# Optimization experiments

Measured on AMD Instinct MI355X. Metric: run time of the kernel, lower is better.

## Reference

```python
import jax, jax.numpy as jnp
import numpy as np

TWO_PI = 2.0 * np.pi


def _grid_sample(w, g):
    """Bilinear sample. w: [M,C,H,W]; g: [M,2,H,W] coords in [-1,1] (x,y),
    align_corners=True, border-clamped."""
    H, W = w.shape[-2], w.shape[-1]
    x = (g[:, 0] + 1.0) * 0.5 * (W - 1)  # [M,H,W]
    y = (g[:, 1] + 1.0) * 0.5 * (H - 1)
    x0 = jnp.floor(x)
    y0 = jnp.floor(y)
    fx = x - x0
    fy = y - y0
    x0i = jnp.clip(x0.astype(jnp.int32), 0, W - 1)
    x1i = jnp.clip(x0i + 1, 0, W - 1)
    y0i = jnp.clip(y0.astype(jnp.int32), 0, H - 1)
    y1i = jnp.clip(y0i + 1, 0, H - 1)

    def samp(wm, yi, xi):
        return wm[:, yi, xi]  # [C,H,W]

    v00 = jax.vmap(samp)(w, y0i, x0i)
    v01 = jax.vmap(samp)(w, y0i, x1i)
    v10 = jax.vmap(samp)(w, y1i, x0i)
    v11 = jax.vmap(samp)(w, y1i, x1i)
    fx = fx[:, None]  # broadcast over channel dim
    fy = fy[:, None]
    return (1 - fy) * ((1 - fx) * v00 + fx * v01) + fy * ((1 - fx) * v10 + fx * v11)


def _forward(in_H, out_H, weight, grid_H, grid_Rn, mask):
    No, Ni = out_H.shape[0], in_H.shape[0]
    N = grid_H.shape[0]
    Gk, Cout, Cin, kh, kw = weight.shape

    # inverse_H: angles negate; left_apply_to_H: angles add (pairwise)
    out_inv = -out_H  # [No,1]
    theta = (out_inv[:, None, 0] + in_H[None, :, 0]).reshape(-1)  # [No*Ni]

    # interpolate_H: periodic linear interp over uniform angle grid
    step = TWO_PI / N
    pos = jnp.mod(theta, TWO_PI) / step
    i0 = jnp.floor(pos).astype(jnp.int32) % N
    i1 = (i0 + 1) % N
    frac = (pos - jnp.floor(pos))[:, None]
    wflat = weight.reshape(Gk, -1)  # [Gk, Cout*Cin*kh*kw]
    w = (1.0 - frac) * wflat[i0] + frac * wflat[i1]  # [No*Ni, C]
    w = w.reshape(No * Ni, Cin * Cout, kh, kw)

    # left_apply_to_Rn: rotate spatial grid by out_H^{-1}
    ang = out_inv[:, 0]
    c, s = jnp.cos(ang), jnp.sin(ang)
    gx = c[:, None, None] * grid_Rn[0] - s[:, None, None] * grid_Rn[1]
    gy = s[:, None, None] * grid_Rn[0] + c[:, None, None] * grid_Rn[1]
    grids = jnp.stack([gx, gy], axis=1)  # [No,2,kh,kw]
    grids = jnp.repeat(grids, Ni, axis=0)  # repeat_interleave -> [No*Ni,2,kh,kw]

    # interpolate_Rn: bilinear grid sample
    w = _grid_sample(w, grids)  # [No*Ni, Cin*Cout, kh, kw]
    w = w.reshape(No, Ni, Cin, Cout, kh, kw)
    # .transpose(0,3).transpose(1,3) -> [Cout, No, Cin, Ni, kh, kw]
    w = jnp.transpose(w, (3, 0, 2, 1, 4, 5))
    return mask * w


def setup_inputs() -> dict:
    key = jax.random.key(0)
    k1, k2, k3 = jax.random.split(key, 3)
    N, Cout, Cin, ks = 8, 128, 128, 5
    in_H = jax.random.uniform(k1, (N, 1), dtype=jnp.float32) * TWO_PI
    out_H = jax.random.uniform(k2, (N, 1), dtype=jnp.float32) * TWO_PI
    fan_in = Cin * ks * ks
    weight = jax.random.normal(k3, (N, Cout, Cin, ks, ks), dtype=jnp.float32) / np.sqrt(fan_in)
    grid_H = (jnp.arange(N) * (TWO_PI / N)).astype(jnp.float32)
    lin = jnp.linspace(-1.0, 1.0, ks)
    X, Y = jnp.meshgrid(lin, lin, indexing='xy')
    grid_Rn = jnp.stack([X, Y]).astype(jnp.float32)  # [2, ks, ks]
    mask = (X ** 2 + Y ** 2 <= 1.0 + 1e-6).astype(jnp.float32)  # circular mask
    return dict(in_H=in_H, out_H=out_H, weight=weight, grid_H=grid_H,
                grid_Rn=grid_Rn, mask=mask)


def reference(in_H, out_H, weight, grid_H, grid_Rn, mask):
    return _forward(in_H, out_H, weight, grid_H, grid_Rn, mask)
```

## Files before the change

### kernel.cpp

```cpp
#include <hip/hip_runtime.h>
#include <math.h>


#define TWO_PI_F 6.28318530717958647692f

__global__ __launch_bounds__(256) void rotconv_weight_kernel(
    const float* __restrict__ in_H,
    const float* __restrict__ out_H,
    const float* __restrict__ weight,
    const float* __restrict__ grid_Rn,
    const float* __restrict__ mask,
    float* __restrict__ out)
{
    __shared__ __align__(16) float s_tile[256 * 25];
    __shared__ int4   s_off[25];
    __shared__ float4 s_w[25];

    const int t  = threadIdx.x;
    const int bx = blockIdx.x;
    const int vt = bx & 7;
    const int ut = (bx >> 3) & 7;
    const int i  = (bx >> 6) & 7;
    const int o  = bx >> 9;
    const int u0 = ut * 16;
    const int v0 = vt * 16;

    const float ang = -out_H[o];

    const float theta = in_H[i] + ang;
    float m = fmodf(theta, TWO_PI_F);
    if (m < 0.0f) m += TWO_PI_F;
    const float pos  = m * (8.0f / TWO_PI_F);
    const float pf   = floorf(pos);
    const float frac = pos - pf;
    const int g0 = ((int)pf) & 7;
    const int g1 = (g0 + 1) & 7;
    const float om = 1.0f - frac;

    if (t < 25) {
        const int k = t;
        float sthe, cthe;
        sincosf(ang, &sthe, &cthe);
        const float X = grid_Rn[k];
        const float Y = grid_Rn[25 + k];
        const float gx = cthe * X - sthe * Y;
        const float gy = sthe * X + cthe * Y;
        const float x = (gx + 1.0f) * 2.0f;
        const float y = (gy + 1.0f) * 2.0f;
        const float x0f = floorf(x);
        const float y0f = floorf(y);
        const float fx = x - x0f;
        const float fy = y - y0f;
        int x0 = (int)x0f; x0 = x0 < 0 ? 0 : (x0 > 4 ? 4 : x0);
        int y0 = (int)y0f; y0 = y0 < 0 ? 0 : (y0 > 4 ? 4 : y0);
        const int x1 = x0 + 1 > 4 ? 4 : x0 + 1;
        const int y1 = y0 + 1 > 4 ? 4 : y0 + 1;
        const float mk = mask[k];
        s_off[k] = make_int4(y0 * 5 + x0, y0 * 5 + x1, y1 * 5 + x0, y1 * 5 + x1);
        s_w[k] = make_float4(mk * (1.0f - fy) * (1.0f - fx),
                             mk * (1.0f - fy) * fx,
                             mk * fy * (1.0f - fx),
                             mk * fy * fx);
    }

    const size_t b0 = ((size_t)(g0 * 128 + u0) * 128 + v0) * 25;
    const size_t b1 = ((size_t)(g1 * 128 + u0) * 128 + v0) * 25;
    for (int f4 = t; f4 < 1600; f4 += 256) {
        const int chunk = f4 / 100;
        const int off4  = f4 - chunk * 100;
        const size_t a  = (size_t)chunk * 3200 + (size_t)off4 * 4;
        const float4 a0 = *reinterpret_cast<const float4*>(weight + b0 + a);
        const float4 a1 = *reinterpret_cast<const float4*>(weight + b1 + a);
        float4 bl;
        bl.x = om * a0.x + frac * a1.x;
        bl.y = om * a0.y + frac * a1.y;
        bl.z = om * a0.z + frac * a1.z;
        bl.w = om * a0.w + frac * a1.w;
        *reinterpret_cast<float4*>(s_tile + (size_t)f4 * 4) = bl;
    }

    __syncthreads();

    const int uu = t >> 4;
    const int vv = t & 15;
    const float* tp = s_tile + t * 25;
    const size_t ob = ((((size_t)(v0 + vv) * 8 + o) * 128 + (u0 + uu)) * 8 + i) * 25;

#pragma unroll
    for (int k = 0; k < 25; ++k) {
        const int4   of = s_off[k];
        const float4 w  = s_w[k];
        out[ob + k] = w.x * tp[of.x] + w.y * tp[of.y]
                    + w.z * tp[of.z] + w.w * tp[of.w];
    }
}

extern "C" void kernel_launch(void* const* d_in, const int* in_sizes, int n_in,
                              void* d_out, int out_size, void* d_ws, size_t ws_size,
                              hipStream_t stream) {
    const float* in_H    = (const float*)d_in[0];
    const float* out_H   = (const float*)d_in[1];
    const float* weight  = (const float*)d_in[2];
    const float* grid_Rn = (const float*)d_in[4];
    const float* mask    = (const float*)d_in[5];
    float* out = (float*)d_out;

    rotconv_weight_kernel<<<dim3(4096), dim3(256), 0, stream>>>(
        in_H, out_H, weight, grid_Rn, mask, out);
}
```

Measured before the change: 159.2 us.

## Remap output phase so threads own one tap and write contiguous runs

Each thread now handles a single kernel tap k, computing its bilinear offsets and weights in registers instead of using shared-memory tables. Groups of 25 threads then walk the (u,v) runs, so consecutive lanes write consecutive output floats, replacing the old pattern where each thread wrote 25 elements with a 25-float stride. The x1 clamp is folded into the weights so loads are adjacent pairs. Only 250 of 256 threads take part in the output phase, and each run index needs about 26 iterations.

New measurement: 145.1 us. 1.1x faster.

```diff
diff --git a/kernel.cpp b/kernel.cpp
--- a/kernel.cpp
+++ b/kernel.cpp
@@ -13,8 +13,6 @@
     float* __restrict__ out)
 {
     __shared__ __align__(16) float s_tile[256 * 25];
-    __shared__ int4   s_off[25];
-    __shared__ float4 s_w[25];
 
     const int t  = threadIdx.x;
     const int bx = blockIdx.x;
@@ -37,8 +35,11 @@
     const int g1 = (g0 + 1) & 7;
     const float om = 1.0f - frac;
 
-    if (t < 25) {
-        const int k = t;
+    const int grp = t / 25;
+    const int k   = t - grp * 25;
+    int rb0, rb1;
+    float w00, w01, w10, w11;
+    {
         float sthe, cthe;
         sincosf(ang, &sthe, &cthe);
         const float X = grid_Rn[k];
@@ -53,14 +54,17 @@
         const float fy = y - y0f;
         int x0 = (int)x0f; x0 = x0 < 0 ? 0 : (x0 > 4 ? 4 : x0);
         int y0 = (int)y0f; y0 = y0 < 0 ? 0 : (y0 > 4 ? 4 : y0);
-        const int x1 = x0 + 1 > 4 ? 4 : x0 + 1;
         const int y1 = y0 + 1 > 4 ? 4 : y0 + 1;
         const float mk = mask[k];
-        s_off[k] = make_int4(y0 * 5 + x0, y0 * 5 + x1, y1 * 5 + x0, y1 * 5 + x1);
-        s_w[k] = make_float4(mk * (1.0f - fy) * (1.0f - fx),
-                             mk * (1.0f - fy) * fx,
-                             mk * fy * (1.0f - fx),
-                             mk * fy * fx);
+        float wa = mk * (1.0f - fy) * (1.0f - fx);
+        float wb = mk * (1.0f - fy) * fx;
+        float wc = mk * fy * (1.0f - fx);
+        float wd = mk * fy * fx;
+        int xb = x0;
+        if (x0 == 4) { xb = 3; wb += wa; wa = 0.0f; wd += wc; wc = 0.0f; }
+        rb0 = y0 * 5 + xb;
+        rb1 = y1 * 5 + xb;
+        w00 = wa; w01 = wb; w10 = wc; w11 = wd;
     }
 
     const size_t b0 = ((size_t)(g0 * 128 + u0) * 128 + v0) * 25;
@@ -81,17 +85,20 @@
 
     __syncthreads();
 
-    const int uu = t >> 4;
-    const int vv = t & 15;
-    const float* tp = s_tile + t * 25;
-    const size_t ob = ((((size_t)(v0 + vv) * 8 + o) * 128 + (u0 + uu)) * 8 + i) * 25;
-
-#pragma unroll
-    for (int k = 0; k < 25; ++k) {
-        const int4   of = s_off[k];
-        const float4 w  = s_w[k];
-        out[ob + k] = w.x * tp[of.x] + w.y * tp[of.y]
-                    + w.z * tp[of.z] + w.w * tp[of.w];
+    const size_t obase = ((((size_t)v0 * 8 + o) * 128 + u0) * 8 + i) * 25 + k;
+    if (grp < 10) {
+#pragma unroll 4
+        for (int run = grp; run < 256; run += 10) {
+            const int uu = run >> 4;
+            const int vv = run & 15;
+            const float* tp = s_tile + run * 25;
+            const float v00 = tp[rb0];
+            const float v01 = tp[rb0 + 1];
+            const float v10 = tp[rb1];
+            const float v11 = tp[rb1 + 1];
+            out[obase + (size_t)vv * 204800 + (size_t)uu * 200] =
+                w00 * v00 + w01 * v01 + w10 * v10 + w11 * v11;
+        }
     }
 }
 
```
